# Performance work log

Hardware: AMD Instinct MI355X
Metric: run time of the kernel (lower is better)

Reference implementation:

```python
import jax, jax.numpy as jnp
import numpy as np

ALIGN_CORNERS = False  # matches init_kwargs


def setup_inputs() -> dict:
    key = jax.random.key(0)
    k1, k2 = jax.random.split(key)
    features = jax.random.normal(k1, (8, 128, 128, 256), dtype=jnp.float32)
    grid = jax.random.uniform(k2, (8, 16384, 2), dtype=jnp.float32)  # values in [0, 1)
    return {"features": features, "grid": grid}


def reference(features, grid):
    # features: [B, H, W, C] (NHWC), grid: [B, P, 2] with values in [0, 1], last axis (x, y)
    B, H, W, C = features.shape
    # pad H and W by 1 on each side so out-of-range corner taps read zeros
    safe = jnp.pad(features, ((0, 0), (1, 1), (1, 1), (0, 0))).astype(grid.dtype)

    g = grid[..., ::-1]  # reverse last axis -> (y, x) matching (H, W)
    size = jnp.asarray([H, W], dtype=grid.dtype)
    if ALIGN_CORNERS:
        g = g * (size - 1)
    else:
        g = (2.0 * g * size - 1.0) / 2.0

    bounds = jnp.asarray([H + 1, W + 1], dtype=jnp.int32)  # per-axis clip max in padded map
    batch_idx = jnp.arange(B)[:, None]  # [B, 1], broadcasts over P

    def lookup(coords):
        c = jnp.clip(coords.astype(jnp.int32) + 1, 0, bounds)  # shift into padded coords
        return safe[batch_idx, c[..., 0], c[..., 1]]  # [B, P, C]

    g_nw = jnp.floor(g)
    g_ne = g_nw + jnp.asarray([1.0, 0.0], g.dtype)
    g_sw = g_nw + jnp.asarray([0.0, 1.0], g.dtype)
    g_se = g_nw + jnp.asarray([1.0, 1.0], g.dtype)

    one = jnp.asarray([1.0, -1.0], g.dtype)
    w_nw = jnp.prod(g_se - g, axis=-1, keepdims=True)
    w_ne = jnp.prod((g_sw - g) * one, axis=-1, keepdims=True)
    w_sw = jnp.prod((g_ne - g) * -one, axis=-1, keepdims=True)
    w_se = jnp.prod(g - g_nw, axis=-1, keepdims=True)

    result = (lookup(g_nw) * w_nw + lookup(g_ne) * w_ne
              + lookup(g_sw) * w_sw + lookup(g_se) * w_se)
    return result.astype(features.dtype)  # [B, P, C]
```

## Files before the change

### kernel.cpp

```cpp
#include <hip/hip_runtime.h>


constexpr int B = 8, H = 128, W = 128, C = 256, P = 16384;
constexpr int PPW = 4;
constexpr int TS = 32;
constexpr int TPS = W / TS;
constexpr int TPB = TPS * TPS;
constexpr int NT = B * TPB;
constexpr int NPTS = B * P;
constexpr int NBLK = NPTS / (4 * PPW);

typedef float f32x4 __attribute__((ext_vector_type(4)));

__device__ __forceinline__ int tile_of_xy(int b, float gx, float gy) {
    int ix = (int)floorf(gx * (float)W - 0.5f);
    int iy = (int)floorf(gy * (float)H - 0.5f);
    ix = min(max(ix, 0), W - 1);
    iy = min(max(iy, 0), H - 1);
    return b * TPB + (iy / TS) * TPS + (ix / TS);
}

__global__ __launch_bounds__(256) void histo_kernel(
    const float* __restrict__ grid, int* __restrict__ cnt)
{
    __shared__ int h[NT];
    const int tid = threadIdx.x;
    if (tid < NT) h[tid] = 0;
    __syncthreads();
    const int pt0 = (blockIdx.x * 256 + tid) * 2;
    const float4 g = *reinterpret_cast<const float4*>(grid + (size_t)pt0 * 2);
    const int b = pt0 >> 14;
    atomicAdd(&h[tile_of_xy(b, g.x, g.y)], 1);
    atomicAdd(&h[tile_of_xy(b, g.z, g.w)], 1);
    __syncthreads();
    if (tid < NT && h[tid]) atomicAdd(&cnt[tid], h[tid]);
}

__global__ __launch_bounds__(256) void scatter_kernel(
    const float* __restrict__ grid, const int* __restrict__ cnt,
    int* __restrict__ off0, int* __restrict__ perm)
{
    __shared__ int h[NT];
    __shared__ int pre[NT];
    __shared__ int base[NT];
    const int tid = threadIdx.x;
    int cv = 0;
    if (tid < NT) { h[tid] = 0; cv = cnt[tid]; pre[tid] = cv; }
    __syncthreads();

    const int pt0 = (blockIdx.x * 256 + tid) * 2;
    const float4 g = *reinterpret_cast<const float4*>(grid + (size_t)pt0 * 2);
    const int b = pt0 >> 14;
    const int t0 = tile_of_xy(b, g.x, g.y);
    const int t1 = tile_of_xy(b, g.z, g.w);
    const int r0 = atomicAdd(&h[t0], 1);
    const int r1 = atomicAdd(&h[t1], 1);

    #pragma unroll
    for (int off = 1; off < NT; off <<= 1) {
        int v = 0;
        if (tid < NT && tid >= off) v = pre[tid - off];
        __syncthreads();
        if (tid < NT) pre[tid] += v;
        __syncthreads();
    }

    if (tid < NT) {
        const int hh = h[tid];
        base[tid] = (pre[tid] - cv) + (hh ? atomicAdd(&off0[tid], hh) : 0);
    }
    __syncthreads();
    perm[base[t0] + r0] = pt0;
    perm[base[t1] + r1] = pt0 + 1;
}

__global__ __launch_bounds__(256) void point_sample_kernel(
    const float* __restrict__ features,
    const float* __restrict__ grid,
    const int* __restrict__ perm,
    float* __restrict__ out)
{
    const int wave = threadIdx.x >> 6;
    const int lane = threadIdx.x & 63;
    int bid = blockIdx.x;
    bid = (bid & 7) * (NBLK >> 3) + (bid >> 3);
    const int w = bid * 4 + wave;

    const int4 pv = *reinterpret_cast<const int4*>(perm + w * PPW);
    const int ptv[PPW] = {pv.x, pv.y, pv.z, pv.w};
    const int c = lane * 4;

    int   off[PPW][4];
    float wgt[PPW][4];
    #pragma unroll
    for (int k = 0; k < PPW; ++k) {
        const int pt = ptv[k];
        const int b = pt >> 14;
        const float2 g = reinterpret_cast<const float2*>(grid)[pt];
        const float x = g.x * (float)W - 0.5f;
        const float y = g.y * (float)H - 0.5f;
        const float fx = floorf(x), fy = floorf(y);
        const int ix = (int)fx, iy = (int)fy;
        const float frx = x - fx, fry = y - fy;

        const int x0 = min(max(ix, 0), W - 1);
        const int x1 = min(max(ix + 1, 0), W - 1);
        const int y0 = min(max(iy, 0), H - 1);
        const int y1 = min(max(iy + 1, 0), H - 1);
        const float mx0 = (ix >= 0 && ix < W)         ? 1.f : 0.f;
        const float mx1 = (ix + 1 >= 0 && ix + 1 < W) ? 1.f : 0.f;
        const float my0 = (iy >= 0 && iy < H)         ? 1.f : 0.f;
        const float my1 = (iy + 1 >= 0 && iy + 1 < H) ? 1.f : 0.f;

        wgt[k][0] = (1.f - fry) * (1.f - frx) * my0 * mx0;
        wgt[k][1] = (1.f - fry) * frx         * my0 * mx1;
        wgt[k][2] = fry         * (1.f - frx) * my1 * mx0;
        wgt[k][3] = fry         * frx         * my1 * mx1;
        const int fbase = b * (H * W * C) + c;
        off[k][0] = fbase + (y0 * W + x0) * C;
        off[k][1] = fbase + (y0 * W + x1) * C;
        off[k][2] = fbase + (y1 * W + x0) * C;
        off[k][3] = fbase + (y1 * W + x1) * C;
    }

    float4 v[PPW][4];
    #pragma unroll
    for (int k = 0; k < PPW; ++k)
        #pragma unroll
        for (int j = 0; j < 4; ++j)
            v[k][j] = *reinterpret_cast<const float4*>(features + off[k][j]);

    #pragma unroll
    for (int k = 0; k < PPW; ++k) {
        f32x4 acc = (f32x4)0.f;
        #pragma unroll
        for (int j = 0; j < 4; ++j) {
            const float wq = wgt[k][j];
            acc.x += wq * v[k][j].x;
            acc.y += wq * v[k][j].y;
            acc.z += wq * v[k][j].z;
            acc.w += wq * v[k][j].w;
        }
        f32x4* op = reinterpret_cast<f32x4*>(out + (size_t)ptv[k] * C + c);
        __builtin_nontemporal_store(acc, op);
    }
}

__global__ __launch_bounds__(256) void point_sample_direct(
    const float* __restrict__ features,
    const float* __restrict__ grid,
    float* __restrict__ out)
{
    const int wave = threadIdx.x >> 6;
    const int lane = threadIdx.x & 63;
    const int pt = blockIdx.x * 4 + wave;
    const int b = pt >> 14;
    const float2 g = reinterpret_cast<const float2*>(grid)[pt];
    const float x = g.x * (float)W - 0.5f;
    const float y = g.y * (float)H - 0.5f;
    const float fx = floorf(x), fy = floorf(y);
    const int ix = (int)fx, iy = (int)fy;
    const float frx = x - fx, fry = y - fy;
    const float* fb = features + (size_t)b * H * W * C;
    const int c = lane * 4;
    f32x4 acc = (f32x4)0.f;
    #pragma unroll
    for (int dy = 0; dy < 2; ++dy) {
        const int hy = iy + dy;
        const bool vy = (hy >= 0) && (hy < H);
        #pragma unroll
        for (int dx = 0; dx < 2; ++dx) {
            const int wx = ix + dx;
            if (vy && (wx >= 0) && (wx < W)) {
                const float wgt = dy ? (dx ? fry * frx : fry * (1.f - frx))
                                     : (dx ? (1.f - fry) * frx : (1.f - fry) * (1.f - frx));
                const float4 vv = *reinterpret_cast<const float4*>(
                    fb + ((size_t)hy * W + wx) * C + c);
                acc.x += wgt * vv.x; acc.y += wgt * vv.y;
                acc.z += wgt * vv.z; acc.w += wgt * vv.w;
            }
        }
    }
    f32x4* op = reinterpret_cast<f32x4*>(out + (size_t)pt * C + c);
    __builtin_nontemporal_store(acc, op);
}

extern "C" void kernel_launch(void* const* d_in, const int* in_sizes, int n_in,
                              void* d_out, int out_size, void* d_ws, size_t ws_size,
                              hipStream_t stream) {
    const float* features = (const float*)d_in[0];
    const float* grid     = (const float*)d_in[1];
    float* out            = (float*)d_out;

    const size_t need = (size_t)(2 * NT + NPTS) * sizeof(int);
    if (ws_size < need) {
        point_sample_direct<<<NPTS / 4, 256, 0, stream>>>(features, grid, out);
        return;
    }

    int* cnt  = (int*)d_ws;
    int* off0 = cnt + NT;
    int* perm = off0 + NT;

    hipMemsetAsync(cnt, 0, 2 * NT * sizeof(int), stream);
    histo_kernel  <<<NPTS / 512, 256, 0, stream>>>(grid, cnt);
    scatter_kernel<<<NPTS / 512, 256, 0, stream>>>(grid, cnt, off0, perm);
    point_sample_kernel<<<NBLK, 256, 0, stream>>>(features, grid, perm, out);
}
```

Baseline: 54.13 us.

## Replace histogram/scatter passes with single per-batch shared-memory bucket sort

Merges the memset, global histogram and scatter kernels into one kernel that launches a 1024-thread block per batch. Each block counts points per spatial tile in shared memory, does a serial prefix over 16 tiles, and writes the permutation within its batch segment. This removes two launches, a memset and global atomics. In exchange only eight blocks run, so the sort phase has little parallelism across the GPU.

```diff
diff --git a/kernel.cpp b/kernel.cpp
--- a/kernel.cpp
+++ b/kernel.cpp
@@ -6,72 +6,49 @@
 constexpr int TS = 32;
 constexpr int TPS = W / TS;
 constexpr int TPB = TPS * TPS;
-constexpr int NT = B * TPB;
 constexpr int NPTS = B * P;
 constexpr int NBLK = NPTS / (4 * PPW);
 
 typedef float f32x4 __attribute__((ext_vector_type(4)));
 
-__device__ __forceinline__ int tile_of_xy(int b, float gx, float gy) {
+__device__ __forceinline__ int tile16(float gx, float gy) {
     int ix = (int)floorf(gx * (float)W - 0.5f);
     int iy = (int)floorf(gy * (float)H - 0.5f);
     ix = min(max(ix, 0), W - 1);
     iy = min(max(iy, 0), H - 1);
-    return b * TPB + (iy / TS) * TPS + (ix / TS);
+    return (iy / TS) * TPS + (ix / TS);
 }
 
-__global__ __launch_bounds__(256) void histo_kernel(
-    const float* __restrict__ grid, int* __restrict__ cnt)
+__global__ __launch_bounds__(1024) void bucket_sort_kernel(
+    const float* __restrict__ grid, int* __restrict__ perm)
 {
-    __shared__ int h[NT];
-    const int tid = threadIdx.x;
-    if (tid < NT) h[tid] = 0;
-    __syncthreads();
-    const int pt0 = (blockIdx.x * 256 + tid) * 2;
-    const float4 g = *reinterpret_cast<const float4*>(grid + (size_t)pt0 * 2);
-    const int b = pt0 >> 14;
-    atomicAdd(&h[tile_of_xy(b, g.x, g.y)], 1);
-    atomicAdd(&h[tile_of_xy(b, g.z, g.w)], 1);
-    __syncthreads();
-    if (tid < NT && h[tid]) atomicAdd(&cnt[tid], h[tid]);
-}
-
-__global__ __launch_bounds__(256) void scatter_kernel(
-    const float* __restrict__ grid, const int* __restrict__ cnt,
-    int* __restrict__ off0, int* __restrict__ perm)
-{
-    __shared__ int h[NT];
-    __shared__ int pre[NT];
-    __shared__ int base[NT];
-    const int tid = threadIdx.x;
-    int cv = 0;
-    if (tid < NT) { h[tid] = 0; cv = cnt[tid]; pre[tid] = cv; }
+    __shared__ int h[TPB];
+    __shared__ int pre[TPB];
+    const int tid  = threadIdx.x;
+    const int base = blockIdx.x * P;
+    if (tid < TPB) h[tid] = 0;
     __syncthreads();
 
-    const int pt0 = (blockIdx.x * 256 + tid) * 2;
-    const float4 g = *reinterpret_cast<const float4*>(grid + (size_t)pt0 * 2);
-    const int b = pt0 >> 14;
-    const int t0 = tile_of_xy(b, g.x, g.y);
-    const int t1 = tile_of_xy(b, g.z, g.w);
-    const int r0 = atomicAdd(&h[t0], 1);
-    const int r1 = atomicAdd(&h[t1], 1);
-
+    int myTile[16], myRank[16];
+    const float2* g2 = reinterpret_cast<const float2*>(grid);
     #pragma unroll
-    for (int off = 1; off < NT; off <<= 1) {
-        int v = 0;
-        if (tid < NT && tid >= off) v = pre[tid - off];
-        __syncthreads();
-        if (tid < NT) pre[tid] += v;
-        __syncthreads();
-    }
-
-    if (tid < NT) {
-        const int hh = h[tid];
-        base[tid] = (pre[tid] - cv) + (hh ? atomicAdd(&off0[tid], hh) : 0);
+    for (int i = 0; i < 16; ++i) {
+        const int pt = base + i * 1024 + tid;
+        const float2 g = g2[pt];
+        const int t = tile16(g.x, g.y);
+        myTile[i] = t;
+        myRank[i] = atomicAdd(&h[t], 1);
     }
     __syncthreads();
-    perm[base[t0] + r0] = pt0;
-    perm[base[t1] + r1] = pt0 + 1;
+    if (tid == 0) {
+        int acc = 0;
+        #pragma unroll
+        for (int t = 0; t < TPB; ++t) { pre[t] = acc; acc += h[t]; }
+    }
+    __syncthreads();
+    #pragma unroll
+    for (int i = 0; i < 16; ++i)
+        perm[base + pre[myTile[i]] + myRank[i]] = base + i * 1024 + tid;
 }
 
 __global__ __launch_bounds__(256) void point_sample_kernel(
@@ -192,18 +169,14 @@
     const float* grid     = (const float*)d_in[1];
     float* out            = (float*)d_out;
 
-    const size_t need = (size_t)(2 * NT + NPTS) * sizeof(int);
+    const size_t need = (size_t)NPTS * sizeof(int);
     if (ws_size < need) {
         point_sample_direct<<<NPTS / 4, 256, 0, stream>>>(features, grid, out);
         return;
     }
 
-    int* cnt  = (int*)d_ws;
-    int* off0 = cnt + NT;
-    int* perm = off0 + NT;
+    int* perm = (int*)d_ws;
 
-    hipMemsetAsync(cnt, 0, 2 * NT * sizeof(int), stream);
-    histo_kernel  <<<NPTS / 512, 256, 0, stream>>>(grid, cnt);
-    scatter_kernel<<<NPTS / 512, 256, 0, stream>>>(grid, cnt, off0, perm);
+    bucket_sort_kernel <<<B, 1024, 0, stream>>>(grid, perm);
     point_sample_kernel<<<NBLK, 256, 0, stream>>>(features, grid, perm, out);
 }
```

Result: no change. 55.21 us (+2.0%).
